# Performance work log

Hardware: AMD Instinct MI355X
Metric: run time of the kernel (lower is better)

The kernel has to match this reference:

```python
import jax, jax.numpy as jnp
import numpy as np

N_NODES = 100000
N_EDGES = 1600000
IN_F, HID_F, OUT_F = 128, 128, 64


def setup_inputs() -> dict:
    key = jax.random.key(0)
    ks = jax.random.split(key, 8)
    x = jax.random.normal(ks[0], (N_NODES, IN_F), dtype=jnp.float32)
    edge_index = jax.random.randint(ks[1], (2, N_EDGES), 0, N_NODES, dtype=jnp.int64)
    w1 = jax.random.normal(ks[2], (IN_F, HID_F), dtype=jnp.float32) * 0.05
    b1 = jax.random.normal(ks[3], (HID_F,), dtype=jnp.float32) * 0.05
    c1 = jax.random.normal(ks[4], (IN_F, HID_F, 3), dtype=jnp.float32) * 0.01
    w2 = jax.random.normal(ks[5], (HID_F, OUT_F), dtype=jnp.float32) * 0.05
    b2 = jax.random.normal(ks[6], (OUT_F,), dtype=jnp.float32) * 0.05
    c2 = jax.random.normal(ks[7], (IN_F, OUT_F, 3), dtype=jnp.float32) * 0.01
    return {"x": x, "edge_index": edge_index, "w1": w1, "b1": b1, "c1": c1,
            "w2": w2, "b2": b2, "c2": c2}


def _minimal_kan(x, w, b, c):
    # linear term: (N, out)
    lin = x @ w + b
    # polynomial basis (x, x^2, x^3): (N, in, 3)
    basis = jnp.stack([x, x * x, x * x * x], axis=-1)
    # fused contraction over (in, 3); same math as the (N,in,out,3) broadcast-sum
    kan_out = jnp.einsum('nib,iob->no', basis, c)
    return lin + 0.1 * kan_out


def _aggregate(h, source, target, num_nodes):
    # mean over incoming messages, degree clamped at 1
    deg = jax.ops.segment_sum(jnp.ones(source.shape[0], dtype=h.dtype), target,
                              num_segments=num_nodes)
    deg = jnp.maximum(deg, 1.0)
    out = jax.ops.segment_sum(h[source], target, num_segments=num_nodes)
    return out / deg[:, None]


def reference(x, edge_index, w1, b1, c1, w2, b2, c2):
    source, target = edge_index[0], edge_index[1]
    n = x.shape[0]
    h = _minimal_kan(x, w1, b1, c1)
    h = jax.nn.relu(h)
    h = _aggregate(h, source, target, n)
    h = _minimal_kan(h, w2, b2, c2)
    h = _aggregate(h, source, target, n)
    return jax.nn.log_softmax(h, axis=-1)
```

## Files before the change

kernel.cpp:

```cpp
#include <hip/hip_runtime.h>
#include <hip/hip_bf16.h>
#include <math.h>

#define N_NODES 100000
#define N_EDGES 1600000
#define IN_F 128
#define HID_F 128
#define OUT_F 64
#define K_TOT 384
#define XLDS_STRIDE 132

#define BK_BITS 9
#define BK_SIZE 512
#define NBUCK ((N_NODES + BK_SIZE - 1) / BK_SIZE)
#define EPB 4096
#define NBLK_SORT ((N_EDGES + EPB - 1) / EPB)
#define PK_SRC_MASK 0x7fffffu
#define PAD8(d) (((d) + 7) & ~7)

typedef __attribute__((ext_vector_type(8))) short s8v;
typedef __attribute__((ext_vector_type(4))) float f4v;
typedef __attribute__((ext_vector_type(2))) float f2v;

__device__ __forceinline__ short f2bf(float f) {
    __hip_bfloat16 h = __float2bfloat16(f);
    return __builtin_bit_cast(short, h);
}
__device__ __forceinline__ float bfhi2f(unsigned u) {
    return __builtin_bit_cast(float, u & 0xffff0000u);
}
__device__ __forceinline__ float bflo2f(unsigned u) {
    return __builtin_bit_cast(float, u << 16);
}

__global__ __launch_bounds__(256) void fold_weights_bf16(
    const float* __restrict__ w1, const float* __restrict__ c1,
    const float* __restrict__ w2, const float* __restrict__ c2,
    short* __restrict__ Wb1, short* __restrict__ Wb2,
    unsigned* __restrict__ h1d, unsigned* __restrict__ h2u)
{
    if (blockIdx.x == 0) {
        if (threadIdx.x < 32) h1d[(size_t)N_NODES * 32 + threadIdx.x] = 0;
        if (threadIdx.x < 32) h2u[(size_t)N_NODES * 32 + threadIdx.x] = 0;
    }
    int idx = blockIdx.x * 256 + threadIdx.x;
    if (idx < K_TOT * HID_F) {
        int k = idx >> 7, n = idx & 127;
        int p = k >> 7, f = k & 127;
        int si = f * HID_F + n;
        float v = (p == 0) ? (w1[si] + 0.1f * c1[si * 3])
                           : 0.1f * c1[si * 3 + p];
        Wb1[(((k >> 3) * HID_F) + n) * 8 + (k & 7)] = f2bf(v);
    } else {
        idx -= K_TOT * HID_F;
        if (idx < K_TOT * OUT_F) {
            int k = idx >> 6, n = idx & 63;
            int p = k >> 7, f = k & 127;
            int si = f * OUT_F + n;
            float v = (p == 0) ? (w2[si] + 0.1f * c2[si * 3])
                               : 0.1f * c2[si * 3 + p];
            Wb2[(((k >> 3) * OUT_F) + n) * 8 + (k & 7)] = f2bf(v);
        }
    }
}

__global__ __launch_bounds__(256) void bucket_hist(
    const int* __restrict__ tgt, int* __restrict__ bucket_cnt)
{
    __shared__ int h[NBUCK];
    int tid = threadIdx.x;
    for (int i = tid; i < NBUCK; i += 256) h[i] = 0;
    __syncthreads();
    int e0 = blockIdx.x * EPB;
    int n = min(EPB, N_EDGES - e0);
    for (int i = tid; i < n; i += 256)
        atomicAdd(&h[tgt[e0 + i] >> BK_BITS], 1);
    __syncthreads();
    for (int i = tid; i < NBUCK; i += 256)
        if (h[i]) atomicAdd(&bucket_cnt[i], h[i]);
}

__global__ __launch_bounds__(256) void bucket_scan(
    const int* __restrict__ cnt, int* __restrict__ boff, int* __restrict__ bcur)
{
    __shared__ int s[256];
    int tid = threadIdx.x;
    int v = (tid < NBUCK) ? cnt[tid] : 0;
    s[tid] = v;
    __syncthreads();
    for (int o = 1; o < 256; o <<= 1) {
        int t = (tid >= o) ? s[tid - o] : 0;
        __syncthreads();
        s[tid] += t;
        __syncthreads();
    }
    int excl = s[tid] - v;
    if (tid < NBUCK) { boff[tid] = excl; bcur[tid] = excl; }
    if (tid == NBUCK - 1) boff[NBUCK] = excl + v;
}

__global__ __launch_bounds__(256) void bucket_scatter(
    const int* __restrict__ src, const int* __restrict__ tgt,
    int* __restrict__ bcur, unsigned* __restrict__ spk)
{
    __shared__ int h[NBUCK];
    __shared__ int base[NBUCK];
    int tid = threadIdx.x;
    for (int i = tid; i < NBUCK; i += 256) h[i] = 0;
    __syncthreads();
    int e0 = blockIdx.x * EPB;
    int n = min(EPB, N_EDGES - e0);
    for (int i = tid; i < n; i += 256)
        atomicAdd(&h[tgt[e0 + i] >> BK_BITS], 1);
    __syncthreads();
    for (int i = tid; i < NBUCK; i += 256) {
        int c = h[i];
        base[i] = c ? atomicAdd(&bcur[i], c) : 0;
        h[i] = 0;
    }
    __syncthreads();
    for (int i = tid; i < n; i += 256) {
        int t = tgt[e0 + i];
        int b = t >> BK_BITS;
        int pos = base[b] + atomicAdd(&h[b], 1);
        spk[pos] = ((unsigned)(t - (b << BK_BITS)) << 23) | (unsigned)src[e0 + i];
    }
}

__global__ __launch_bounds__(256) void bucket_rowstart(
    const int* __restrict__ boff, const unsigned* __restrict__ spk,
    int* __restrict__ row_start, int* __restrict__ pbsum)
{
    __shared__ int d[BK_SIZE];
    __shared__ int s[256];
    int tid = threadIdx.x;
    int b = blockIdx.x;
    d[tid] = 0; d[tid + 256] = 0;
    __syncthreads();
    int e0 = boff[b], e1 = boff[b + 1];
    for (int i = e0 + tid; i < e1; i += 256)
        atomicAdd(&d[spk[i] >> 23], 1);
    __syncthreads();
    int a0 = d[2 * tid], a1c = d[2 * tid + 1];
    int tsum = a0 + a1c;
    s[tid] = tsum;
    __syncthreads();
    for (int o = 1; o < 256; o <<= 1) {
        int t = (tid >= o) ? s[tid - o] : 0;
        __syncthreads();
        s[tid] += t;
        __syncthreads();
    }
    int excl = s[tid] - tsum;
    int nbase = b << BK_BITS;
    int n0 = nbase + 2 * tid, n1 = n0 + 1;
    int rs0 = e0 + excl;
    if (n0 < N_NODES) row_start[n0] = rs0;
    if (n1 < N_NODES) row_start[n1] = rs0 + a0;
    if (b == NBUCK - 1 && tid == 0) row_start[N_NODES] = boff[NBUCK];

    int pc0 = (n0 < N_NODES) ? PAD8(a0) : 0;
    int pc1 = (n1 < N_NODES) ? PAD8(a1c) : 0;
    __syncthreads();
    s[tid] = pc0 + pc1;
    __syncthreads();
    for (int o = 128; o > 0; o >>= 1) {
        if (tid < o) s[tid] += s[tid + o];
        __syncthreads();
    }
    if (tid == 0) pbsum[b] = s[0];
}

__global__ __launch_bounds__(256) void bucket_prow(
    const int* __restrict__ row_start, const int* __restrict__ pboff,
    int* __restrict__ prow)
{
    __shared__ int s[256];
    int tid = threadIdx.x;
    int b = blockIdx.x;
    int nbase = b << BK_BITS;
    int n0 = nbase + 2 * tid, n1 = n0 + 1;
    int d0 = (n0 < N_NODES) ? row_start[n0 + 1] - row_start[n0] : 0;
    int d1 = (n1 < N_NODES) ? row_start[n1 + 1] - row_start[n1] : 0;
    int pc0 = (n0 < N_NODES) ? PAD8(d0) : 0;
    int pc1 = (n1 < N_NODES) ? PAD8(d1) : 0;
    int tsum = pc0 + pc1;
    s[tid] = tsum;
    __syncthreads();
    for (int o = 1; o < 256; o <<= 1) {
        int t = (tid >= o) ? s[tid - o] : 0;
        __syncthreads();
        s[tid] += t;
        __syncthreads();
    }
    int excl = s[tid] - tsum;
    int base = pboff[b] + excl;
    if (n0 < N_NODES) prow[n0] = base;
    if (n1 < N_NODES) prow[n1] = base + pc0;
    if (b == NBUCK - 1 && tid == 0) prow[N_NODES] = pboff[NBUCK];
}

__global__ __launch_bounds__(256) void csr_fine_pad(
    const int* __restrict__ boff, const unsigned* __restrict__ spk,
    const int* __restrict__ prow, int* __restrict__ csr_pad)
{
    __shared__ int cur[BK_SIZE];
    int tid = threadIdx.x;
    int b = blockIdx.x;
    int nbase = b << BK_BITS;
    for (int i = tid; i < BK_SIZE; i += 256) {
        int nd = nbase + i;
        cur[i] = (nd < N_NODES) ? prow[nd] : 0;
    }
    __syncthreads();
    int e0 = boff[b], e1 = boff[b + 1];
    for (int i = e0 + tid; i < e1; i += 256) {
        unsigned pk = spk[i];
        int pos = atomicAdd(&cur[pk >> 23], 1);
        csr_pad[pos] = (int)(pk & PK_SRC_MASK);
    }
    __syncthreads();
    for (int i = tid; i < BK_SIZE; i += 256) {
        int nd = nbase + i;
        if (nd < N_NODES) {
            int kend = prow[nd + 1];
            for (int k = cur[i]; k < kend; ++k) csr_pad[k] = N_NODES;
        }
    }
}

__global__ __launch_bounds__(256) void kan1_mfma(
    const float* __restrict__ x, const short* __restrict__ Wb,
    const float* __restrict__ bias, unsigned* __restrict__ h1d)
{
    __shared__ float sx[64 * XLDS_STRIDE];
    const int tid  = threadIdx.x;
    const int lane = tid & 63;
    const int wave = tid >> 6;
    const int node0 = blockIdx.x * 64;
    const int q = lane >> 4, r = lane & 15;

#pragma unroll
    for (int it = 0; it < 8; ++it) {
        int idx = tid + 256 * it;
        int m = idx >> 5, c4 = (idx & 31) * 4;
        int gm = min(node0 + m, N_NODES - 1);
        float4 v = *(const float4*)(x + (size_t)gm * IN_F + c4);
        *(float4*)(sx + m * XLDS_STRIDE + c4) = v;
    }
    __syncthreads();

    const int wm = (wave & 1) * 32;
    const int wn = (wave >> 1) * 64;

    f4v acc[2][4];
#pragma unroll
    for (int i = 0; i < 2; ++i)
#pragma unroll
        for (int j = 0; j < 4; ++j)
            acc[i][j] = (f4v){0.f, 0.f, 0.f, 0.f};

    float bj[4];
#pragma unroll
    for (int j = 0; j < 4; ++j) bj[j] = bias[wn + j * 16 + r];

#pragma unroll
    for (int kb = 0; kb < 12; ++kb) {
        const int p  = kb >> 2;
        const int f0 = (kb & 3) * 32 + q * 8;

        s8v afrag[2];
#pragma unroll
        for (int i = 0; i < 2; ++i) {
            const float* xs = sx + (wm + i * 16 + r) * XLDS_STRIDE + f0;
            float4 v0 = *(const float4*)xs;
            float4 v1 = *(const float4*)(xs + 4);
            float v[8] = {v0.x, v0.y, v0.z, v0.w, v1.x, v1.y, v1.z, v1.w};
            s8v a;
#pragma unroll
            for (int t = 0; t < 8; ++t) {
                float e = v[t];
                if (p >= 1) e *= v[t];
                if (p == 2) e *= v[t];
                a[t] = f2bf(e);
            }
            afrag[i] = a;
        }
#pragma unroll
        for (int j = 0; j < 4; ++j) {
            const s8v b = *(const s8v*)(Wb + (((kb * 4 + q) * HID_F) + wn + j * 16 + r) * 8);
            acc[0][j] = __builtin_amdgcn_mfma_f32_16x16x32_bf16(afrag[0], b, acc[0][j], 0, 0, 0);
            acc[1][j] = __builtin_amdgcn_mfma_f32_16x16x32_bf16(afrag[1], b, acc[1][j], 0, 0, 0);
        }
    }

    const int dci = ((wn >> 6) << 4) + r;
#pragma unroll
    for (int i = 0; i < 2; ++i)
#pragma unroll
        for (int e = 0; e < 4; ++e) {
            int grow = node0 + wm + i * 16 + q * 4 + e;
            if (grow < N_NODES) {
                float v0 = fmaxf(acc[i][0][e] + bj[0], 0.f);
                float v1 = fmaxf(acc[i][1][e] + bj[1], 0.f);
                float v2 = fmaxf(acc[i][2][e] + bj[2], 0.f);
                float v3 = fmaxf(acc[i][3][e] + bj[3], 0.f);
                int pk = __builtin_amdgcn_cvt_pk_fp8_f32(v0, v1, 0, false);
                pk = __builtin_amdgcn_cvt_pk_fp8_f32(v2, v3, pk, true);
                h1d[(size_t)grow * 32 + dci] = (unsigned)pk;
            }
        }
}

__global__ __launch_bounds__(256) void gather128(
    const unsigned* __restrict__ h1d, const int* __restrict__ prow,
    const int* __restrict__ csr_pad, unsigned short* __restrict__ a1s)
{
    const int lane  = threadIdx.x & 63;
    const int wave  = threadIdx.x >> 6;
    const int hl    = lane & 31;
    const int half  = lane >> 5;
    const int hbase = half << 5;
    const int node  = blockIdx.x * 8 + wave * 2 + half;

    int p0 = prow[node], p1 = prow[node + 1];
    int cnt = p1 - p0;
    int cmax = max(cnt, __shfl_xor(cnt, 32));

    float acc[4][4];
#pragma unroll
    for (int t = 0; t < 4; ++t)
#pragma unroll
        for (int b = 0; b < 4; ++b) acc[t][b] = 0.f;

    for (int base = 0; base < cmax; base += 32) {
        int idx = max(min(p0 + base + hl, p1 - 1), 0);
        int sreg = csr_pad[idx];
        int lim = min(32, cmax - base);
        for (int j = 0; j < lim; j += 4) {
            if (base + j < cnt) {
                unsigned u[4];
#pragma unroll
                for (int t = 0; t < 4; ++t) {
                    int sj = __shfl(sreg, hbase + j + t);
                    u[t] = h1d[(size_t)sj * 32 + hl];
                }
#pragma unroll
                for (int t = 0; t < 4; ++t) {
                    f2v lo = __builtin_amdgcn_cvt_pk_f32_fp8(u[t], false);
                    f2v hi = __builtin_amdgcn_cvt_pk_f32_fp8(u[t], true);
                    acc[t][0] += lo.x; acc[t][1] += lo.y;
                    acc[t][2] += hi.x; acc[t][3] += hi.y;
                }
            }
        }
    }

    const int r  = hl & 15;
    const int jj = hl >> 4;
    size_t obase = (size_t)node * 128 + (jj << 6) + r;
#pragma unroll
    for (int b = 0; b < 4; ++b) {
        float s = (acc[0][b] + acc[1][b]) + (acc[2][b] + acc[3][b]);
        a1s[obase + (b << 4)] = (unsigned short)f2bf(s);
    }
}

__global__ __launch_bounds__(256) void kan2_mfma(
    const unsigned* __restrict__ a1u, const int* __restrict__ row_start,
    const short* __restrict__ Wb, const float* __restrict__ bias,
    short* __restrict__ h2)
{
    __shared__ float sx[64 * XLDS_STRIDE];
    const int tid  = threadIdx.x;
    const int lane = tid & 63;
    const int wave = tid >> 6;
    const int node0 = blockIdx.x * 64;
    const int q = lane >> 4, r = lane & 15;

    const uint2* a1v = (const uint2*)a1u;
#pragma unroll
    for (int it = 0; it < 8; ++it) {
        int idx = tid + 256 * it;
        int m = idx >> 5, c2 = idx & 31;
        int gm = min(node0 + m, N_NODES - 1);
        float di = 1.0f / fmaxf((float)(row_start[gm + 1] - row_start[gm]), 1.0f);
        uint2 u = a1v[(size_t)gm * 32 + c2];
        float4 v;
        v.x = bflo2f(u.x) * di; v.y = bfhi2f(u.x) * di;
        v.z = bflo2f(u.y) * di; v.w = bfhi2f(u.y) * di;
        *(float4*)(sx + m * XLDS_STRIDE + 4 * c2) = v;
    }
    __syncthreads();

    const int wm = (wave & 1) * 32;
    const int wn = (wave >> 1) * 32;

    f4v acc[2][2];
#pragma unroll
    for (int i = 0; i < 2; ++i)
#pragma unroll
        for (int j = 0; j < 2; ++j)
            acc[i][j] = (f4v){0.f, 0.f, 0.f, 0.f};

    float bj[2];
#pragma unroll
    for (int j = 0; j < 2; ++j) bj[j] = bias[wn + j * 16 + r];

#pragma unroll
    for (int kb = 0; kb < 12; ++kb) {
        const int p  = kb >> 2;
        const int f0 = (kb & 3) * 32 + q * 8;

        s8v afrag[2];
#pragma unroll
        for (int i = 0; i < 2; ++i) {
            const float* xs = sx + (wm + i * 16 + r) * XLDS_STRIDE + f0;
            float4 v0 = *(const float4*)xs;
            float4 v1 = *(const float4*)(xs + 4);
            float v[8] = {v0.x, v0.y, v0.z, v0.w, v1.x, v1.y, v1.z, v1.w};
            s8v a;
#pragma unroll
            for (int t = 0; t < 8; ++t) {
                float e = v[t];
                if (p >= 1) e *= v[t];
                if (p == 2) e *= v[t];
                a[t] = f2bf(e);
            }
            afrag[i] = a;
        }
#pragma unroll
        for (int j = 0; j < 2; ++j) {
            const s8v b = *(const s8v*)(Wb + (((kb * 4 + q) * OUT_F) + wn + j * 16 + r) * 8);
            acc[0][j] = __builtin_amdgcn_mfma_f32_16x16x32_bf16(afrag[0], b, acc[0][j], 0, 0, 0);
            acc[1][j] = __builtin_amdgcn_mfma_f32_16x16x32_bf16(afrag[1], b, acc[1][j], 0, 0, 0);
        }
    }

#pragma unroll
    for (int i = 0; i < 2; ++i)
#pragma unroll
        for (int j = 0; j < 2; ++j)
#pragma unroll
            for (int e = 0; e < 4; ++e) {
                int grow = node0 + wm + i * 16 + q * 4 + e;
                if (grow < N_NODES) {
                    int gcol = wn + j * 16 + r;
                    h2[(size_t)grow * OUT_F + gcol] = f2bf(acc[i][j][e] + bj[j]);
                }
            }
}

__global__ __launch_bounds__(256) void gather64_lsm(
    const unsigned* __restrict__ h2u, const int* __restrict__ row_start,
    const int* __restrict__ prow, const int* __restrict__ csr_pad,
    float* __restrict__ out)
{
    const int lane = threadIdx.x & 63;
    const int wave = threadIdx.x >> 6;
    const int hl   = lane & 31;
    const int half = lane >> 5;
    const int node = blockIdx.x * 8 + wave * 2 + half;

    int p0 = prow[node], p1 = prow[node + 1];
    int cnt = p1 - p0;
    int degr = row_start[node + 1] - row_start[node];
    int cmax = max(cnt, __shfl_xor(cnt, 32));

    float alo[8], ahi[8];
#pragma unroll
    for (int t = 0; t < 8; ++t) { alo[t] = 0.f; ahi[t] = 0.f; }

    for (int base = 0; base < cmax; base += 32) {
        int idx = max(min(p0 + base + hl, p1 - 1), 0);
        int sreg = csr_pad[idx];
        int lim = min(32, cmax - base);
        for (int j = 0; j < lim; j += 8) {
            if (base + j < cnt) {
                unsigned u[8];
#pragma unroll
                for (int t = 0; t < 8; ++t) {
                    int sj = __shfl(sreg, (half << 5) + j + t);
                    u[t] = h2u[(size_t)sj * 32 + hl];
                }
#pragma unroll
                for (int t = 0; t < 8; ++t) {
                    alo[t] += bflo2f(u[t]);
                    ahi[t] += bfhi2f(u[t]);
                }
            }
        }
    }
    float slo = ((alo[0] + alo[1]) + (alo[2] + alo[3])) + ((alo[4] + alo[5]) + (alo[6] + alo[7]));
    float shi = ((ahi[0] + ahi[1]) + (ahi[2] + ahi[3])) + ((ahi[4] + ahi[5]) + (ahi[6] + ahi[7]));

    float di = 1.0f / fmaxf((float)degr, 1.0f);
    float vlo = slo * di, vhi = shi * di;

    float m = fmaxf(vlo, vhi);
#pragma unroll
    for (int off = 16; off >= 1; off >>= 1)
        m = fmaxf(m, __shfl_xor(m, off));
    float e = expf(vlo - m) + expf(vhi - m);
#pragma unroll
    for (int off = 16; off >= 1; off >>= 1)
        e += __shfl_xor(e, off);
    float ls = logf(e);
    float2 o; o.x = vlo - m - ls; o.y = vhi - m - ls;
    *(float2*)(out + (size_t)node * OUT_F + 2 * hl) = o;
}

extern "C" void kernel_launch(void* const* d_in, const int* in_sizes, int n_in,
                              void* d_out, int out_size, void* d_ws, size_t ws_size,
                              hipStream_t stream)
{
    const float* x  = (const float*)d_in[0];
    const int*   ei = (const int*)d_in[1];
    const float* w1 = (const float*)d_in[2];
    const float* b1 = (const float*)d_in[3];
    const float* c1 = (const float*)d_in[4];
    const float* w2 = (const float*)d_in[5];
    const float* b2 = (const float*)d_in[6];
    const float* c2 = (const float*)d_in[7];
    float* out = (float*)d_out;

    const int* src = ei;
    const int* tgt = ei + N_EDGES;

    char* ws = (char*)d_ws;
    size_t off = 0;
    auto carve = [&](size_t bytes) -> void* {
        void* p = ws + off;
        off = (off + bytes + 255) & ~(size_t)255;
        return p;
    };
    short*    Wb1       = (short*)carve((size_t)K_TOT * HID_F * 2);
    short*    Wb2       = (short*)carve((size_t)K_TOT * OUT_F * 2);
    int*      row_start = (int*)carve(((size_t)N_NODES + 1) * 4);
    int*      prow      = (int*)carve(((size_t)N_NODES + 1) * 4);
    int*      bucket_cnt= (int*)carve((size_t)NBUCK * 4);
    int*      boff      = (int*)carve(((size_t)NBUCK + 1) * 4);
    int*      bcur      = (int*)carve((size_t)NBUCK * 4);
    int*      pbsum     = (int*)carve((size_t)NBUCK * 4);
    int*      pboff     = (int*)carve(((size_t)NBUCK + 1) * 4);
    int*      pbcur     = (int*)carve((size_t)NBUCK * 4);
    unsigned* spk       = (unsigned*)carve((size_t)N_EDGES * 4);
    int*      csr_pad   = (int*)carve(((size_t)N_EDGES + 7 * (size_t)N_NODES + 64) * 4);
    unsigned* h1d       = (unsigned*)carve(((size_t)N_NODES + 1) * 128);
    unsigned* a1u       = (unsigned*)carve((size_t)N_NODES * 64 * 4);
    short*    h2        = (short*)carve(((size_t)N_NODES + 1) * OUT_F * 2);

    const int grid_mm = (N_NODES + 63) / 64;

    hipMemsetAsync(bucket_cnt, 0, (size_t)NBUCK * 4, stream);
    bucket_hist<<<NBLK_SORT, 256, 0, stream>>>(tgt, bucket_cnt);
    bucket_scan<<<1, 256, 0, stream>>>(bucket_cnt, boff, bcur);
    bucket_scatter<<<NBLK_SORT, 256, 0, stream>>>(src, tgt, bcur, spk);
    bucket_rowstart<<<NBUCK, 256, 0, stream>>>(boff, spk, row_start, pbsum);
    bucket_scan<<<1, 256, 0, stream>>>(pbsum, pboff, pbcur);
    bucket_prow<<<NBUCK, 256, 0, stream>>>(row_start, pboff, prow);
    csr_fine_pad<<<NBUCK, 256, 0, stream>>>(boff, spk, prow, csr_pad);

    fold_weights_bf16<<<(K_TOT * HID_F + K_TOT * OUT_F + 255) / 256, 256, 0, stream>>>(
        w1, c1, w2, c2, Wb1, Wb2, h1d, (unsigned*)h2);
    kan1_mfma<<<grid_mm, 256, 0, stream>>>(x, Wb1, b1, h1d);

    gather128<<<(N_NODES + 7) / 8, 256, 0, stream>>>(
        h1d, prow, csr_pad, (unsigned short*)a1u);

    kan2_mfma<<<grid_mm, 256, 0, stream>>>(a1u, row_start, Wb2, b2, h2);

    gather64_lsm<<<(N_NODES + 7) / 8, 256, 0, stream>>>(
        (const unsigned*)h2, row_start, prow, csr_pad, out);
}
```

Measured before the change: 283.2 us.

## Store aggregated and layer-2 activations in fp8 and fuse CSR finalize kernels

```diff
diff --git a/kernel.cpp b/kernel.cpp
--- a/kernel.cpp
+++ b/kernel.cpp
@@ -37,11 +37,11 @@
     const float* __restrict__ w1, const float* __restrict__ c1,
     const float* __restrict__ w2, const float* __restrict__ c2,
     short* __restrict__ Wb1, short* __restrict__ Wb2,
-    unsigned* __restrict__ h1d, unsigned* __restrict__ h2u)
+    unsigned* __restrict__ h1d, unsigned* __restrict__ h2d)
 {
     if (blockIdx.x == 0) {
         if (threadIdx.x < 32) h1d[(size_t)N_NODES * 32 + threadIdx.x] = 0;
-        if (threadIdx.x < 32) h2u[(size_t)N_NODES * 32 + threadIdx.x] = 0;
+        if (threadIdx.x < 16) h2d[(size_t)N_NODES * 16 + threadIdx.x] = 0;
     }
     int idx = blockIdx.x * 256 + threadIdx.x;
     if (idx < K_TOT * HID_F) {
@@ -171,13 +171,29 @@
     if (tid == 0) pbsum[b] = s[0];
 }
 
-__global__ __launch_bounds__(256) void bucket_prow(
-    const int* __restrict__ row_start, const int* __restrict__ pboff,
-    int* __restrict__ prow)
+__global__ __launch_bounds__(256) void csr_finalize(
+    const int* __restrict__ boff, const unsigned* __restrict__ spk,
+    const int* __restrict__ row_start, const int* __restrict__ pbsum,
+    int* __restrict__ prow, int* __restrict__ csr_pad)
 {
     __shared__ int s[256];
+    __shared__ int cur[BK_SIZE];
     int tid = threadIdx.x;
     int b = blockIdx.x;
+
+    int v = (tid < NBUCK) ? pbsum[tid] : 0;
+    s[tid] = v;
+    __syncthreads();
+    for (int o = 1; o < 256; o <<= 1) {
+        int t = (tid >= o) ? s[tid - o] : 0;
+        __syncthreads();
+        s[tid] += t;
+        __syncthreads();
+    }
+    int pboff_b = (b > 0) ? s[b - 1] : 0;
+    int ptotal  = s[NBUCK - 1];
+    __syncthreads();
+
     int nbase = b << BK_BITS;
     int n0 = nbase + 2 * tid, n1 = n0 + 1;
     int d0 = (n0 < N_NODES) ? row_start[n0 + 1] - row_start[n0] : 0;
@@ -194,25 +210,12 @@
         __syncthreads();
     }
     int excl = s[tid] - tsum;
-    int base = pboff[b] + excl;
-    if (n0 < N_NODES) prow[n0] = base;
-    if (n1 < N_NODES) prow[n1] = base + pc0;
-    if (b == NBUCK - 1 && tid == 0) prow[N_NODES] = pboff[NBUCK];
-}
-
-__global__ __launch_bounds__(256) void csr_fine_pad(
-    const int* __restrict__ boff, const unsigned* __restrict__ spk,
-    const int* __restrict__ prow, int* __restrict__ csr_pad)
-{
-    __shared__ int cur[BK_SIZE];
-    int tid = threadIdx.x;
-    int b = blockIdx.x;
-    int nbase = b << BK_BITS;
-    for (int i = tid; i < BK_SIZE; i += 256) {
-        int nd = nbase + i;
-        cur[i] = (nd < N_NODES) ? prow[nd] : 0;
-    }
-    __syncthreads();
+    int base = pboff_b + excl;
+    if (n0 < N_NODES) { prow[n0] = base;       cur[2 * tid]     = base; }
+    if (n1 < N_NODES) { prow[n1] = base + pc0; cur[2 * tid + 1] = base + pc0; }
+    if (b == NBUCK - 1 && tid == 0) prow[N_NODES] = ptotal;
+    __syncthreads();
+
     int e0 = boff[b], e1 = boff[b + 1];
     for (int i = e0 + tid; i < e1; i += 256) {
         unsigned pk = spk[i];
@@ -220,10 +223,11 @@
         csr_pad[pos] = (int)(pk & PK_SRC_MASK);
     }
     __syncthreads();
+
     for (int i = tid; i < BK_SIZE; i += 256) {
         int nd = nbase + i;
         if (nd < N_NODES) {
-            int kend = prow[nd + 1];
+            int kend = prow[nd] + PAD8(row_start[nd + 1] - row_start[nd]);
             for (int k = cur[i]; k < kend; ++k) csr_pad[k] = N_NODES;
         }
     }
@@ -314,7 +318,7 @@
 
 __global__ __launch_bounds__(256) void gather128(
     const unsigned* __restrict__ h1d, const int* __restrict__ prow,
-    const int* __restrict__ csr_pad, unsigned short* __restrict__ a1s)
+    const int* __restrict__ csr_pad, unsigned* __restrict__ a1d)
 {
     const int lane  = threadIdx.x & 63;
     const int wave  = threadIdx.x >> 6;
@@ -356,20 +360,19 @@
         }
     }
 
-    const int r  = hl & 15;
-    const int jj = hl >> 4;
-    size_t obase = (size_t)node * 128 + (jj << 6) + r;
-#pragma unroll
-    for (int b = 0; b < 4; ++b) {
-        float s = (acc[0][b] + acc[1][b]) + (acc[2][b] + acc[3][b]);
-        a1s[obase + (b << 4)] = (unsigned short)f2bf(s);
-    }
+    float s0 = (acc[0][0] + acc[1][0]) + (acc[2][0] + acc[3][0]);
+    float s1 = (acc[0][1] + acc[1][1]) + (acc[2][1] + acc[3][1]);
+    float s2 = (acc[0][2] + acc[1][2]) + (acc[2][2] + acc[3][2]);
+    float s3 = (acc[0][3] + acc[1][3]) + (acc[2][3] + acc[3][3]);
+    int pk = __builtin_amdgcn_cvt_pk_fp8_f32(s0, s1, 0, false);
+    pk = __builtin_amdgcn_cvt_pk_fp8_f32(s2, s3, pk, true);
+    a1d[(size_t)node * 32 + hl] = (unsigned)pk;
 }
 
 __global__ __launch_bounds__(256) void kan2_mfma(
-    const unsigned* __restrict__ a1u, const int* __restrict__ row_start,
+    const unsigned* __restrict__ a1d, const int* __restrict__ row_start,
     const short* __restrict__ Wb, const float* __restrict__ bias,
-    short* __restrict__ h2)
+    unsigned short* __restrict__ h2s)
 {
     __shared__ float sx[64 * XLDS_STRIDE];
     const int tid  = threadIdx.x;
@@ -378,18 +381,20 @@
     const int node0 = blockIdx.x * 64;
     const int q = lane >> 4, r = lane & 15;
 
-    const uint2* a1v = (const uint2*)a1u;
 #pragma unroll
     for (int it = 0; it < 8; ++it) {
         int idx = tid + 256 * it;
-        int m = idx >> 5, c2 = idx & 31;
+        int m = idx >> 5, c = idx & 31;
         int gm = min(node0 + m, N_NODES - 1);
         float di = 1.0f / fmaxf((float)(row_start[gm + 1] - row_start[gm]), 1.0f);
-        uint2 u = a1v[(size_t)gm * 32 + c2];
-        float4 v;
-        v.x = bflo2f(u.x) * di; v.y = bfhi2f(u.x) * di;
-        v.z = bflo2f(u.y) * di; v.w = bfhi2f(u.y) * di;
-        *(float4*)(sx + m * XLDS_STRIDE + 4 * c2) = v;
+        unsigned u = a1d[(size_t)gm * 32 + c];
+        f2v lo = __builtin_amdgcn_cvt_pk_f32_fp8(u, false);
+        f2v hi = __builtin_amdgcn_cvt_pk_f32_fp8(u, true);
+        float* row = sx + m * XLDS_STRIDE + (((c >> 4) << 6) + (c & 15));
+        row[0]  = lo.x * di;
+        row[16] = lo.y * di;
+        row[32] = hi.x * di;
+        row[48] = hi.y * di;
     }
     __syncthreads();
 
@@ -437,22 +442,23 @@
         }
     }
 
+    const int s = (wn >> 1) + r;
 #pragma unroll
     for (int i = 0; i < 2; ++i)
 #pragma unroll
-        for (int j = 0; j < 2; ++j)
-#pragma unroll
-            for (int e = 0; e < 4; ++e) {
-                int grow = node0 + wm + i * 16 + q * 4 + e;
-                if (grow < N_NODES) {
-                    int gcol = wn + j * 16 + r;
-                    h2[(size_t)grow * OUT_F + gcol] = f2bf(acc[i][j][e] + bj[j]);
-                }
+        for (int e = 0; e < 4; ++e) {
+            int grow = node0 + wm + i * 16 + q * 4 + e;
+            if (grow < N_NODES) {
+                float vlo = acc[i][0][e] + bj[0];
+                float vhi = acc[i][1][e] + bj[1];
+                int pk = __builtin_amdgcn_cvt_pk_fp8_f32(vlo, vhi, 0, false);
+                h2s[(size_t)grow * 32 + s] = (unsigned short)(pk & 0xffff);
             }
+        }
 }
 
 __global__ __launch_bounds__(256) void gather64_lsm(
-    const unsigned* __restrict__ h2u, const int* __restrict__ row_start,
+    const unsigned short* __restrict__ h2s, const int* __restrict__ row_start,
     const int* __restrict__ prow, const int* __restrict__ csr_pad,
     float* __restrict__ out)
 {
@@ -477,16 +483,16 @@
         int lim = min(32, cmax - base);
         for (int j = 0; j < lim; j += 8) {
             if (base + j < cnt) {
-                unsigned u[8];
+                int u[8];
 #pragma unroll
                 for (int t = 0; t < 8; ++t) {
                     int sj = __shfl(sreg, (half << 5) + j + t);
-                    u[t] = h2u[(size_t)sj * 32 + hl];
+                    u[t] = (int)h2s[(size_t)sj * 32 + hl];
                 }
 #pragma unroll
                 for (int t = 0; t < 8; ++t) {
-                    alo[t] += bflo2f(u[t]);
-                    ahi[t] += bfhi2f(u[t]);
+                    alo[t] += __builtin_amdgcn_cvt_f32_fp8(u[t], 0);
+                    ahi[t] += __builtin_amdgcn_cvt_f32_fp8(u[t], 1);
                 }
             }
         }
@@ -506,8 +512,10 @@
     for (int off = 16; off >= 1; off >>= 1)
         e += __shfl_xor(e, off);
     float ls = logf(e);
-    float2 o; o.x = vlo - m - ls; o.y = vhi - m - ls;
-    *(float2*)(out + (size_t)node * OUT_F + 2 * hl) = o;
+
+    const int f_lo = ((hl >> 4) << 5) + (hl & 15);
+    out[(size_t)node * OUT_F + f_lo]      = vlo - m - ls;
+    out[(size_t)node * OUT_F + f_lo + 16] = vhi - m - ls;
 }
 
 extern "C" void kernel_launch(void* const* d_in, const int* in_sizes, int n_in,
@@ -542,13 +550,11 @@
     int*      boff      = (int*)carve(((size_t)NBUCK + 1) * 4);
     int*      bcur      = (int*)carve((size_t)NBUCK * 4);
     int*      pbsum     = (int*)carve((size_t)NBUCK * 4);
-    int*      pboff     = (int*)carve(((size_t)NBUCK + 1) * 4);
-    int*      pbcur     = (int*)carve((size_t)NBUCK * 4);
     unsigned* spk       = (unsigned*)carve((size_t)N_EDGES * 4);
     int*      csr_pad   = (int*)carve(((size_t)N_EDGES + 7 * (size_t)N_NODES + 64) * 4);
     unsigned* h1d       = (unsigned*)carve(((size_t)N_NODES + 1) * 128);
-    unsigned* a1u       = (unsigned*)carve((size_t)N_NODES * 64 * 4);
-    short*    h2        = (short*)carve(((size_t)N_NODES + 1) * OUT_F * 2);
+    unsigned* a1d       = (unsigned*)carve((size_t)N_NODES * 128);
+    unsigned short* h2s = (unsigned short*)carve(((size_t)N_NODES + 1) * 64);
 
     const int grid_mm = (N_NODES + 63) / 64;
 
@@ -557,19 +563,16 @@
     bucket_scan<<<1, 256, 0, stream>>>(bucket_cnt, boff, bcur);
     bucket_scatter<<<NBLK_SORT, 256, 0, stream>>>(src, tgt, bcur, spk);
     bucket_rowstart<<<NBUCK, 256, 0, stream>>>(boff, spk, row_start, pbsum);
-    bucket_scan<<<1, 256, 0, stream>>>(pbsum, pboff, pbcur);
-    bucket_prow<<<NBUCK, 256, 0, stream>>>(row_start, pboff, prow);
-    csr_fine_pad<<<NBUCK, 256, 0, stream>>>(boff, spk, prow, csr_pad);
+    csr_finalize<<<NBUCK, 256, 0, stream>>>(boff, spk, row_start, pbsum, prow, csr_pad);
 
     fold_weights_bf16<<<(K_TOT * HID_F + K_TOT * OUT_F + 255) / 256, 256, 0, stream>>>(
-        w1, c1, w2, c2, Wb1, Wb2, h1d, (unsigned*)h2);
+        w1, c1, w2, c2, Wb1, Wb2, h1d, (unsigned*)h2s);
     kan1_mfma<<<grid_mm, 256, 0, stream>>>(x, Wb1, b1, h1d);
 
-    gather128<<<(N_NODES + 7) / 8, 256, 0, stream>>>(
-        h1d, prow, csr_pad, (unsigned short*)a1u);
-
-    kan2_mfma<<<grid_mm, 256, 0, stream>>>(a1u, row_start, Wb2, b2, h2);
+    gather128<<<(N_NODES + 7) / 8, 256, 0, stream>>>(h1d, prow, csr_pad, a1d);
+
+    kan2_mfma<<<grid_mm, 256, 0, stream>>>(a1d, row_start, Wb2, b2, h2s);
 
     gather64_lsm<<<(N_NODES + 7) / 8, 256, 0, stream>>>(
-        (const unsigned*)h2, row_start, prow, csr_pad, out);
-}
+        h2s, row_start, prow, csr_pad, out);
+}
```

New measurement: 274.6 us. 1.03x faster.
